# Optimization experiments

Hardware: AMD Instinct MI355X
Metric: run time of the kernel (lower is better)

Reference implementation:

```python
import jax, jax.numpy as jnp
import numpy as np

BN_EPS = 1e-5

def setup_inputs() -> dict:
    key = jax.random.key(0)
    k1, k2 = jax.random.split(key)
    B, C, H, W, K = 256, 2048, 7, 7, 16
    featmap = jax.random.normal(k1, (B, C, H, W), dtype=jnp.float32)
    w16 = jax.random.normal(k2, (K, C), dtype=jnp.float32) * 0.02  # 1x1 conv weight
    bn_gamma = jnp.ones((K,), jnp.float32)
    bn_beta = jnp.zeros((K,), jnp.float32)
    bn_mean = jnp.zeros((K,), jnp.float32)
    bn_var = jnp.ones((K,), jnp.float32)
    return {"featmap": featmap, "w16": w16, "bn_gamma": bn_gamma,
            "bn_beta": bn_beta, "bn_mean": bn_mean, "bn_var": bn_var}

def reference(featmap, w16, bn_gamma, bn_beta, bn_mean, bn_var):
    # featmap: [B, 2048, 7, 7]; 1x1 conv -> featcov16: [B, 16, 7, 7]
    featcov16 = jnp.einsum('bchw,kc->bkhw', featmap, w16)
    # BatchNorm2d(16), inference-style with running stats
    inv = bn_gamma / jnp.sqrt(bn_var + BN_EPS)
    featcov16 = featcov16 * inv[None, :, None, None] + (bn_beta - bn_mean * inv)[None, :, None, None]
    # Loop-free bilinear pooling: original repeats featcov16[:,i] to 2048 ch,
    # multiplies with featmap, and AvgPool2d(7) -> mean over HxW.
    HW = featmap.shape[2] * featmap.shape[3]
    feat_matrix = jnp.einsum('bkhw,bchw->bkc', featcov16, featmap) / HW  # [B,16,2048]
    bp_out_feat = feat_matrix.reshape(feat_matrix.shape[0], -1)  # [B, 32768]
    return bp_out_feat
```

## Files before the change

### kernel.cpp

```cpp
#include <hip/hip_runtime.h>

#define BATCH 256
#define CDIM  2048
#define HW    49
#define KDIM  16
#define CHUNK 512
#define TILE  128

__global__ __launch_bounds__(256) void pconv_kernel(
    const float* __restrict__ fm, const float* __restrict__ w16,
    float* __restrict__ Ppart)
{
    __shared__ __align__(16) float fm_t[6304];

    const int tid = threadIdx.x;
    const int b   = blockIdx.x >> 2;
    const int q   = blockIdx.x & 3;
    const int hw  = tid & 63;
    const int wv  = __builtin_amdgcn_readfirstlane(tid >> 6);

    float acc[16];
    #pragma unroll
    for (int k = 0; k < 16; ++k) acc[k] = 0.f;

    const float* fmb = fm + (size_t)b * CDIM * HW;

    for (int tile = 0; tile < 4; ++tile) {
        const int ct = q * CHUNK + tile * TILE;
        __syncthreads();
        const float4* src = (const float4*)(fmb + ct * HW);
        float4* dst = (float4*)fm_t;
        #pragma unroll
        for (int it = 0; it < 6; ++it) dst[it * 256 + tid] = src[it * 256 + tid];
        if (tid < 32) dst[1536 + tid] = src[1536 + tid];
        __syncthreads();

        const float* wbase = w16 + ct + wv * 32;
        #pragma unroll 2
        for (int j4 = 0; j4 < 8; ++j4) {
            const int cc = wv * 32 + j4 * 4;
            float f0 = fm_t[(cc + 0) * HW + hw];
            float f1 = fm_t[(cc + 1) * HW + hw];
            float f2 = fm_t[(cc + 2) * HW + hw];
            float f3 = fm_t[(cc + 3) * HW + hw];
            #pragma unroll
            for (int k = 0; k < 16; ++k) {
                const float4 wq = *(const float4*)(wbase + k * CDIM + j4 * 4);
                acc[k] += wq.x * f0 + wq.y * f1 + wq.z * f2 + wq.w * f3;
            }
        }
    }

    __syncthreads();
    float* red = fm_t;
    #pragma unroll
    for (int k = 0; k < 16; ++k) red[wv * 1088 + hw * 17 + k] = acc[k];
    __syncthreads();

    const int e = tid * 4;
    if (e < 784) {
        float4 o;
        #pragma unroll
        for (int j = 0; j < 4; ++j) {
            const int ee = e + j, hh = ee >> 4, kk = ee & 15;
            ((float*)&o)[j] = red[hh * 17 + kk] + red[1088 + hh * 17 + kk]
                            + red[2176 + hh * 17 + kk] + red[3264 + hh * 17 + kk];
        }
        *(float4*)(Ppart + (size_t)blockIdx.x * 784 + e) = o;
    }
}

__global__ __launch_bounds__(256) void preduce_kernel(
    const float* __restrict__ Ppart,
    const float* __restrict__ gamma, const float* __restrict__ beta,
    const float* __restrict__ mean, const float* __restrict__ var,
    float* __restrict__ Pbn)
{
    const int b = blockIdx.x;
    const float* pp = Ppart + (size_t)b * 4 * 784;
    for (int p = threadIdx.x; p < 784; p += 256) {
        float s = pp[p] + pp[p + 784] + pp[p + 1568] + pp[p + 2352];
        const int kk = p & 15;
        float inv   = gamma[kk] * rsqrtf(var[kk] + 1e-5f);
        float shift = beta[kk] - mean[kk] * inv;
        Pbn[(size_t)b * 784 + p] = (s * inv + shift) * (1.0f / 49.0f);
    }
}

__global__ __launch_bounds__(256) void bp_kernel(
    const float* __restrict__ fm, const float* __restrict__ Pbn,
    float* __restrict__ out)
{
    __shared__ __align__(16) float fm_s[256 * HW];

    const int tid = threadIdx.x;
    const int b   = blockIdx.x >> 3;
    const int c0  = (blockIdx.x & 7) * 256;

    const float4* src = (const float4*)(fm + ((size_t)b * CDIM + c0) * HW);
    float4* dst = (float4*)fm_s;
    #pragma unroll
    for (int i = 0; i < 12; ++i) dst[i * 256 + tid] = src[i * 256 + tid];
    if (tid < 64) dst[3072 + tid] = src[3072 + tid];
    __syncthreads();

    const float* Pb = Pbn + (size_t)b * 784;

    float acc[16];
    #pragma unroll
    for (int i = 0; i < 16; ++i) acc[i] = 0.f;

    const float* row = fm_s + tid * HW;
    #pragma unroll 7
    for (int hw = 0; hw < HW; ++hw) {
        float f = row[hw];
        const float4 p0 = *(const float4*)(Pb + hw * 16 + 0);
        const float4 p1 = *(const float4*)(Pb + hw * 16 + 4);
        const float4 p2 = *(const float4*)(Pb + hw * 16 + 8);
        const float4 p3 = *(const float4*)(Pb + hw * 16 + 12);
        acc[0]  += p0.x * f; acc[1]  += p0.y * f; acc[2]  += p0.z * f; acc[3]  += p0.w * f;
        acc[4]  += p1.x * f; acc[5]  += p1.y * f; acc[6]  += p1.z * f; acc[7]  += p1.w * f;
        acc[8]  += p2.x * f; acc[9]  += p2.y * f; acc[10] += p2.z * f; acc[11] += p2.w * f;
        acc[12] += p3.x * f; acc[13] += p3.y * f; acc[14] += p3.z * f; acc[15] += p3.w * f;
    }

    float* ob = out + (size_t)b * (KDIM * CDIM) + c0 + tid;
    #pragma unroll
    for (int kk = 0; kk < 16; ++kk) ob[kk * CDIM] = acc[kk];
}

extern "C" void kernel_launch(void* const* d_in, const int* in_sizes, int n_in,
                              void* d_out, int out_size, void* d_ws, size_t ws_size,
                              hipStream_t stream) {
    const float* fm    = (const float*)d_in[0];
    const float* w16   = (const float*)d_in[1];
    const float* gamma = (const float*)d_in[2];
    const float* beta  = (const float*)d_in[3];
    const float* mean  = (const float*)d_in[4];
    const float* var   = (const float*)d_in[5];
    float* out   = (float*)d_out;
    float* Ppart = (float*)d_ws;
    float* Pbn   = Ppart + (size_t)1024 * 784;

    pconv_kernel<<<BATCH * 4, 256, 0, stream>>>(fm, w16, Ppart);
    preduce_kernel<<<BATCH, 256, 0, stream>>>(Ppart, gamma, beta, mean, var, Pbn);
    bp_kernel<<<BATCH * 8, 256, 0, stream>>>(fm, Pbn, out);
}
```

Measured before the change: 219.8 us.

## Load featmap directly from global in pconv and register-stage bp rows

The pconv kernel no longer stages 128-channel featmap tiles in shared memory with two barriers per tile. Each wave now reads its own 128 channels straight from global memory, one lane per spatial position, with 15 of 64 lanes idle. The cross-wave reduction uses an unpadded float4 layout so the partial sums can be read back as vectors. In bp_kernel each thread copies its 49-element row from LDS into registers before a fully unrolled loop, which raises register pressure and may lower occupancy; the stride-49 row reads may also cause LDS bank conflicts.

Result: slower. 227.8 us (+3.6%).

```diff
diff --git a/kernel.cpp b/kernel.cpp
--- a/kernel.cpp
+++ b/kernel.cpp
@@ -4,68 +4,62 @@
 #define CDIM  2048
 #define HW    49
 #define KDIM  16
-#define CHUNK 512
-#define TILE  128
 
 __global__ __launch_bounds__(256) void pconv_kernel(
     const float* __restrict__ fm, const float* __restrict__ w16,
     float* __restrict__ Ppart)
 {
-    __shared__ __align__(16) float fm_t[6304];
+    __shared__ __align__(16) float red[4 * 784];
 
-    const int tid = threadIdx.x;
-    const int b   = blockIdx.x >> 2;
-    const int q   = blockIdx.x & 3;
-    const int hw  = tid & 63;
-    const int wv  = __builtin_amdgcn_readfirstlane(tid >> 6);
+    const int tid  = threadIdx.x;
+    const int lane = tid & 63;
+    const int wv   = __builtin_amdgcn_readfirstlane(tid >> 6);
+    const int b    = blockIdx.x >> 2;
+    const int q    = blockIdx.x & 3;
 
     float acc[16];
     #pragma unroll
     for (int k = 0; k < 16; ++k) acc[k] = 0.f;
 
-    const float* fmb = fm + (size_t)b * CDIM * HW;
-
-    for (int tile = 0; tile < 4; ++tile) {
-        const int ct = q * CHUNK + tile * TILE;
-        __syncthreads();
-        const float4* src = (const float4*)(fmb + ct * HW);
-        float4* dst = (float4*)fm_t;
-        #pragma unroll
-        for (int it = 0; it < 6; ++it) dst[it * 256 + tid] = src[it * 256 + tid];
-        if (tid < 32) dst[1536 + tid] = src[1536 + tid];
-        __syncthreads();
-
-        const float* wbase = w16 + ct + wv * 32;
+    if (lane < HW) {
+        const float* fmb = fm + (size_t)b * CDIM * HW + lane;
+        const int cbase = q * 512 + wv * 128;
         #pragma unroll 2
-        for (int j4 = 0; j4 < 8; ++j4) {
-            const int cc = wv * 32 + j4 * 4;
-            float f0 = fm_t[(cc + 0) * HW + hw];
-            float f1 = fm_t[(cc + 1) * HW + hw];
-            float f2 = fm_t[(cc + 2) * HW + hw];
-            float f3 = fm_t[(cc + 3) * HW + hw];
+        for (int c4 = 0; c4 < 128; c4 += 4) {
+            const int cg = cbase + c4;
+            float f0 = fmb[(cg + 0) * HW];
+            float f1 = fmb[(cg + 1) * HW];
+            float f2 = fmb[(cg + 2) * HW];
+            float f3 = fmb[(cg + 3) * HW];
             #pragma unroll
             for (int k = 0; k < 16; ++k) {
-                const float4 wq = *(const float4*)(wbase + k * CDIM + j4 * 4);
+                const float4 wq = *(const float4*)(w16 + k * CDIM + cg);
                 acc[k] += wq.x * f0 + wq.y * f1 + wq.z * f2 + wq.w * f3;
             }
         }
     }
 
+    if (lane < HW) {
+        #pragma unroll
+        for (int k4 = 0; k4 < 4; ++k4) {
+            float4 v;
+            v.x = acc[k4 * 4 + 0]; v.y = acc[k4 * 4 + 1];
+            v.z = acc[k4 * 4 + 2]; v.w = acc[k4 * 4 + 3];
+            *(float4*)&red[wv * 784 + lane * 16 + k4 * 4] = v;
+        }
+    }
     __syncthreads();
-    float* red = fm_t;
-    #pragma unroll
-    for (int k = 0; k < 16; ++k) red[wv * 1088 + hw * 17 + k] = acc[k];
-    __syncthreads();
-
-    const int e = tid * 4;
-    if (e < 784) {
+    if (tid < 196) {
+        const int e = tid * 4;
+        float4 a0 = *(const float4*)&red[e];
+        float4 a1 = *(const float4*)&red[784 + e];
+        float4 a2 = *(const float4*)&red[1568 + e];
+        float4 a3 = *(const float4*)&red[2352 + e];
         float4 o;
-        #pragma unroll
-        for (int j = 0; j < 4; ++j) {
-            const int ee = e + j, hh = ee >> 4, kk = ee & 15;
-            ((float*)&o)[j] = red[hh * 17 + kk] + red[1088 + hh * 17 + kk]
-                            + red[2176 + hh * 17 + kk] + red[3264 + hh * 17 + kk];
-        }
+        o.x = a0.x + a1.x + a2.x + a3.x;
+        o.y = a0.y + a1.y + a2.y + a3.y;
+        o.z = a0.z + a1.z + a2.z + a3.z;
+        o.w = a0.w + a1.w + a2.w + a3.w;
         *(float4*)(Ppart + (size_t)blockIdx.x * 784 + e) = o;
     }
 }
@@ -104,24 +98,27 @@
     if (tid < 64) dst[3072 + tid] = src[3072 + tid];
     __syncthreads();
 
+    float f[HW];
+    #pragma unroll
+    for (int i = 0; i < HW; ++i) f[i] = fm_s[tid * HW + i];
+
     const float* Pb = Pbn + (size_t)b * 784;
 
     float acc[16];
     #pragma unroll
     for (int i = 0; i < 16; ++i) acc[i] = 0.f;
 
-    const float* row = fm_s + tid * HW;
-    #pragma unroll 7
+    #pragma unroll
     for (int hw = 0; hw < HW; ++hw) {
-        float f = row[hw];
         const float4 p0 = *(const float4*)(Pb + hw * 16 + 0);
         const float4 p1 = *(const float4*)(Pb + hw * 16 + 4);
         const float4 p2 = *(const float4*)(Pb + hw * 16 + 8);
         const float4 p3 = *(const float4*)(Pb + hw * 16 + 12);
-        acc[0]  += p0.x * f; acc[1]  += p0.y * f; acc[2]  += p0.z * f; acc[3]  += p0.w * f;
-        acc[4]  += p1.x * f; acc[5]  += p1.y * f; acc[6]  += p1.z * f; acc[7]  += p1.w * f;
-        acc[8]  += p2.x * f; acc[9]  += p2.y * f; acc[10] += p2.z * f; acc[11] += p2.w * f;
-        acc[12] += p3.x * f; acc[13] += p3.y * f; acc[14] += p3.z * f; acc[15] += p3.w * f;
+        const float fv = f[hw];
+        acc[0]  += p0.x * fv; acc[1]  += p0.y * fv; acc[2]  += p0.z * fv; acc[3]  += p0.w * fv;
+        acc[4]  += p1.x * fv; acc[5]  += p1.y * fv; acc[6]  += p1.z * fv; acc[7]  += p1.w * fv;
+        acc[8]  += p2.x * fv; acc[9]  += p2.y * fv; acc[10] += p2.z * fv; acc[11] += p2.w * fv;
+        acc[12] += p3.x * fv; acc[13] += p3.y * fv; acc[14] += p3.z * fv; acc[15] += p3.w * fv;
     }
 
     float* ob = out + (size_t)b * (KDIM * CDIM) + c0 + tid;
```
